# Performance work log

Measured on AMD Instinct MI355X. Metric: run time of the kernel, lower is better.

The kernel has to match this reference:

```python
import jax, jax.numpy as jnp
import numpy as np

N_EMBD = 64
N_HEAD = 8
HEAD_SIZE = N_EMBD // N_HEAD  # 8
BLOCK_SIZE = 64
B = 4096
SCALE = N_EMBD ** (-0.5)  # NOTE: source scales by C**-0.5 with C=n_embd, not head_size
EPS = 1e-5


def setup_inputs() -> dict:
    key = jax.random.key(0)
    ks = jax.random.split(key, 12)
    s = 0.02
    return {
        "x": jax.random.normal(ks[0], (B, BLOCK_SIZE, N_EMBD), jnp.float32),
        # per-head q/k/v projections packed as [C, H, hs] (no bias in source)
        "Wq": jax.random.normal(ks[1], (N_EMBD, N_HEAD, HEAD_SIZE), jnp.float32) * s,
        "Wk": jax.random.normal(ks[2], (N_EMBD, N_HEAD, HEAD_SIZE), jnp.float32) * s,
        "Wv": jax.random.normal(ks[3], (N_EMBD, N_HEAD, HEAD_SIZE), jnp.float32) * s,
        "Wo": jax.random.normal(ks[4], (N_EMBD, N_EMBD), jnp.float32) * s,
        "bo": jnp.zeros((N_EMBD,), jnp.float32),
        "W1": jax.random.normal(ks[5], (N_EMBD, 4 * N_EMBD), jnp.float32) * s,
        "b1": jnp.zeros((4 * N_EMBD,), jnp.float32),
        "W2": jax.random.normal(ks[6], (4 * N_EMBD, N_EMBD), jnp.float32) * s,
        "b2": jnp.zeros((N_EMBD,), jnp.float32),
        "g1": jnp.ones((N_EMBD,), jnp.float32),
        "be1": jnp.zeros((N_EMBD,), jnp.float32),
        "g2": jnp.ones((N_EMBD,), jnp.float32),
        "be2": jnp.zeros((N_EMBD,), jnp.float32),
    }


def _layernorm(x, g, b):
    mu = jnp.mean(x, axis=-1, keepdims=True)
    var = jnp.mean(jnp.square(x - mu), axis=-1, keepdims=True)
    return (x - mu) * jax.lax.rsqrt(var + EPS) * g + b


def reference(x, Wq, Wk, Wv, Wo, bo, W1, b1, W2, b2, g1, be1, g2, be2):
    Bb, T, C = x.shape
    # --- multi-head causal self-attention (dropout = identity in eval) ---
    h = _layernorm(x, g1, be1)
    q = jnp.einsum('btc,chd->bhtd', h, Wq)
    k = jnp.einsum('btc,chd->bhtd', h, Wk)
    v = jnp.einsum('btc,chd->bhtd', h, Wv)
    wei = jnp.einsum('bhtd,bhsd->bhts', q, k) * SCALE
    mask = jnp.tril(jnp.ones((T, T), dtype=bool))
    wei = jnp.where(mask, wei, -jnp.inf)
    wei = jax.nn.softmax(wei, axis=-1)
    attn = jnp.einsum('bhts,bhsd->bhtd', wei, v)
    attn = attn.transpose(0, 2, 1, 3).reshape(Bb, T, C)  # concat heads
    x = x + attn @ Wo + bo
    # --- feed-forward ---
    h2 = _layernorm(x, g2, be2)
    ff = jax.nn.relu(h2 @ W1 + b1) @ W2 + b2
    return x + ff
```

## Files before the change

### kernel.cpp

```cpp
#include <hip/hip_runtime.h>
#include <hip/hip_bf16.h>


typedef __attribute__((ext_vector_type(8))) short short8;
typedef __attribute__((ext_vector_type(4))) float f32x4;

#if __has_builtin(__builtin_amdgcn_exp2f)
#define EXP2F(x) __builtin_amdgcn_exp2f(x)
#else
#define EXP2F(x) __expf((x) * 0.69314718056f)
#endif
#if __has_builtin(__builtin_amdgcn_rcpf)
#define RCPF(x) __builtin_amdgcn_rcpf(x)
#else
#define RCPF(x) (1.0f / (x))
#endif

#define ST  72
#define STU 136
#define OH  0
#define OKK 4608
#define OV  9216
#define OP  13896
#define OU  4608
#define NSH 18504

__device__ __forceinline__ short f2bf(float f) {
    unsigned int u = __float_as_uint(f);
    u += 0x7fffu + ((u >> 16) & 1u);
    return (short)(u >> 16);
}
__device__ __forceinline__ unsigned pk2(float a, float b) {
    float2 t; t.x = a; t.y = b;
    __hip_bfloat162 h = __float22bfloat162_rn(t);
    unsigned u; __builtin_memcpy(&u, &h, 4); return u;
}
__device__ __forceinline__ f32x4 mfma16(short8 a, short8 b, f32x4 c) {
    return __builtin_amdgcn_mfma_f32_16x16x32_bf16(a, b, c, 0, 0, 0);
}

__global__ __launch_bounds__(64) void prepack_kernel(
    const float* __restrict__ Wq, const float* __restrict__ Wk,
    const float* __restrict__ Wv, const float* __restrict__ Wo,
    const float* __restrict__ W1, const float* __restrict__ W2,
    short* __restrict__ ws)
{
    int gid = blockIdx.x * 64 + threadIdx.x;
    int lane = gid & 63;
    int fid  = gid >> 6;
    int quad = lane >> 4, nn = lane & 15;
    short8 o;
    if (fid < 24) {
        int tile = fid >> 1, ks = fid & 1;
        const float* Ws = (tile < 4) ? Wq : ((tile < 8) ? Wk : Wv);
        float scale = (tile < 4) ? 0.18033688011f : 1.0f;
        int col = (tile & 3) * 16 + nn;
#pragma unroll
        for (int j = 0; j < 8; ++j)
            o[j] = f2bf(Ws[(ks * 32 + quad * 8 + j) * 64 + col] * scale);
    } else if (fid < 32) {
        int idx = fid - 24, nt = idx >> 1, ks = idx & 1;
#pragma unroll
        for (int j = 0; j < 8; ++j)
            o[j] = f2bf(Wo[(ks * 32 + quad * 8 + j) * 64 + nt * 16 + nn]);
    } else if (fid < 64) {
        int idx = fid - 32, c = idx >> 3, tile = (idx >> 1) & 3, ks = idx & 1;
#pragma unroll
        for (int j = 0; j < 8; ++j)
            o[j] = f2bf(W1[(ks * 32 + quad * 8 + j) * 256 + c * 64 + tile * 16 + nn]);
    } else {
        int idx = fid - 64, c = idx >> 3, nt = (idx >> 1) & 3, ks = idx & 1;
#pragma unroll
        for (int j = 0; j < 8; ++j)
            o[j] = f2bf(W2[(c * 64 + ks * 32 + quad * 8 + j) * 64 + nt * 16 + nn]);
    }
    *(short8*)(ws + (size_t)gid * 8) = o;
}

__global__ __launch_bounds__(256, 4) void block_kernel(
    const float* __restrict__ x,
    const float* __restrict__ bo,
    const float* __restrict__ b1,
    const float* __restrict__ b2,
    const float* __restrict__ g1, const float* __restrict__ be1,
    const float* __restrict__ g2, const float* __restrict__ be2,
    const short8* __restrict__ WB,
    float* __restrict__ out)
{
    __shared__ short sm[NSH];
    const int tid  = threadIdx.x;
    const int wv   = tid >> 6;
    const int lane = tid & 63;
    const int quad = lane >> 4;
    const int nn   = lane & 15;
    const int t_my = wv * 16 + nn;
    const int b    = blockIdx.x;
    const float* xb = x + (size_t)b * 4096;
    const f32x4 zf = {0.f, 0.f, 0.f, 0.f};
    const short8 z8 = {0, 0, 0, 0, 0, 0, 0, 0};

    if (tid < ST) sm[OV + 64 * ST + tid] = (short)0x3F80;
    float xr[16];
    float gv[4], bv[4];
#pragma unroll
    for (int nt = 0; nt < 4; ++nt) { gv[nt] = g1[nt * 16 + nn]; bv[nt] = be1[nt * 16 + nn]; }
#pragma unroll
    for (int nt = 0; nt < 4; ++nt)
#pragma unroll
        for (int r = 0; r < 4; ++r)
            xr[nt * 4 + r] = xb[(wv * 16 + quad * 4 + r) * 64 + nt * 16 + nn];
#pragma unroll
    for (int r = 0; r < 4; ++r) {
        float s1 = 0.f, s2 = 0.f;
#pragma unroll
        for (int nt = 0; nt < 4; ++nt) { float v = xr[nt * 4 + r]; s1 += v; s2 += v * v; }
        s1 += __shfl_xor(s1, 1); s1 += __shfl_xor(s1, 2); s1 += __shfl_xor(s1, 4); s1 += __shfl_xor(s1, 8);
        s2 += __shfl_xor(s2, 1); s2 += __shfl_xor(s2, 2); s2 += __shfl_xor(s2, 4); s2 += __shfl_xor(s2, 8);
        float mu = s1 * 0.015625f;
        float rstd = rsqrtf(s2 * 0.015625f - mu * mu + 1e-5f);
        int base = OH + (wv * 16 + quad * 4 + r) * ST + nn;
        float h0 = (xr[0 + r]  - mu) * rstd * gv[0] + bv[0];
        float h1 = (xr[4 + r]  - mu) * rstd * gv[1] + bv[1];
        float h2 = (xr[8 + r]  - mu) * rstd * gv[2] + bv[2];
        float h3 = (xr[12 + r] - mu) * rstd * gv[3] + bv[3];
        unsigned pA = pk2(h0, h1), pB = pk2(h2, h3);
        sm[base +  0] = (short)pA;
        sm[base + 16] = (short)(pA >> 16);
        sm[base + 32] = (short)pB;
        sm[base + 48] = (short)(pB >> 16);
    }
    __syncthreads();

    unsigned qp[8];
    {
        const short8 wk0 = WB[(size_t)((4 + wv) * 2 + 0) * 64 + lane];
        const short8 wk1 = WB[(size_t)((4 + wv) * 2 + 1) * 64 + lane];
        const short8 wv0 = WB[(size_t)((8 + wv) * 2 + 0) * 64 + lane];
        const short8 wv1 = WB[(size_t)((8 + wv) * 2 + 1) * 64 + lane];
        short8 hf0 = *(const short8*)&sm[OH + t_my * ST + quad * 8];
        short8 hf1 = *(const short8*)&sm[OH + t_my * ST + 32 + quad * 8];
#pragma unroll
        for (int jt = 0; jt < 4; ++jt) {
            f32x4 a = mfma16(WB[(size_t)(jt * 2 + 0) * 64 + lane], hf0, zf);
            a = mfma16(WB[(size_t)(jt * 2 + 1) * 64 + lane], hf1, a);
            qp[jt * 2 + 0] = pk2(a[0], a[1]);
            qp[jt * 2 + 1] = pk2(a[2], a[3]);
        }
#pragma unroll
        for (int rt = 0; rt < 4; ++rt) {
            short8 hA = *(const short8*)&sm[OH + (rt * 16 + nn) * ST + quad * 8];
            short8 hB = *(const short8*)&sm[OH + (rt * 16 + nn) * ST + 32 + quad * 8];
            f32x4 ka = mfma16(wk0, hA, zf); ka = mfma16(wk1, hB, ka);
            uint2 w1; w1.x = pk2(ka[0], ka[1]); w1.y = pk2(ka[2], ka[3]);
            *(uint2*)&sm[OKK + (rt * 16 + nn) * ST + wv * 16 + quad * 4] = w1;
            f32x4 va = mfma16(hA, wv0, zf); va = mfma16(hB, wv1, va);
            uint2 w2; w2.x = pk2(va[0], va[1]); w2.y = pk2(va[2], va[3]);
            *(uint2*)&sm[OV + (wv * 16 + nn) * ST + rt * 16 + quad * 4] = w2;
        }
    }
    __syncthreads();

    const bool keep0 = (quad * 4 + 0) <= nn, keep1 = (quad * 4 + 1) <= nn;
    const bool keep2 = (quad * 4 + 2) <= nn, keep3 = (quad * 4 + 3) <= nn;
    const int arow_base = (nn < 8) ? nn : 64;
    const int arow_step = (nn < 8) ? 8 : 0;
    const int nks = (wv < 2) ? 1 : 2;
    const int zhi = nks * 2;
    for (int mt = wv + 1; mt < zhi; ++mt) {
        uint2 w; w.x = 0u; w.y = 0u;
        *(uint2*)&sm[OP + t_my * ST + mt * 16 + quad * 4] = w;
    }
#pragma unroll 2
    for (int h = 0; h < 8; ++h) {
        short8 bq;
        {
            int qsA = ((h & 1) * 2) * 16 + nn, qsB = qsA + 16;
            int qi = (h >> 1) * 2;
            union { unsigned u[4]; short8 s; } bb;
            bb.u[0] = __shfl(qp[qi + 0], qsA);
            bb.u[1] = __shfl(qp[qi + 1], qsA);
            bb.u[2] = __shfl(qp[qi + 0], qsB);
            bb.u[3] = __shfl(qp[qi + 1], qsB);
            bq = bb.s;
        }
#pragma unroll
        for (int mt = 0; mt < 4; ++mt) {
            if (mt <= wv) {
                short8 ak = z8;
                if (quad == 0) ak = *(const short8*)&sm[OKK + (mt * 16 + nn) * ST + h * 8];
                f32x4 s = mfma16(ak, bq, zf);
                float e0 = EXP2F(s[0]), e1 = EXP2F(s[1]), e2 = EXP2F(s[2]), e3 = EXP2F(s[3]);
                if (mt == wv) {
                    e0 = keep0 ? e0 : 0.f; e1 = keep1 ? e1 : 0.f;
                    e2 = keep2 ? e2 : 0.f; e3 = keep3 ? e3 : 0.f;
                }
                uint2 w; w.x = pk2(e0, e1); w.y = pk2(e2, e3);
                *(uint2*)&sm[OP + t_my * ST + mt * 16 + quad * 4] = w;
            }
        }
        const int arow = arow_base + h * arow_step;
        f32x4 pv = zf;
#pragma unroll
        for (int ks = 0; ks < 2; ++ks) {
            if (ks < nks) {
                short8 av = *(const short8*)&sm[OV + arow * ST + ks * 32 + quad * 8];
                short8 bp = *(const short8*)&sm[OP + t_my * ST + ks * 32 + quad * 8];
                pv = mfma16(av, bp, pv);
            }
        }
        float denom = __shfl(pv[0], 32 + nn);
        float rd = RCPF(denom);
        if (quad < 2) {
            uint2 w; w.x = pk2(pv[0] * rd, pv[1] * rd); w.y = pk2(pv[2] * rd, pv[3] * rd);
            *(uint2*)&sm[OH + t_my * ST + h * 8 + quad * 4] = w;
        }
    }

    {
        short8 aa0 = *(const short8*)&sm[OH + t_my * ST + quad * 8];
        short8 aa1 = *(const short8*)&sm[OH + t_my * ST + 32 + quad * 8];
#pragma unroll
        for (int nt = 0; nt < 4; ++nt) {
            f32x4 oa = mfma16(aa0, WB[(size_t)(24 + nt * 2 + 0) * 64 + lane], zf);
            oa = mfma16(aa1, WB[(size_t)(24 + nt * 2 + 1) * 64 + lane], oa);
            float bov = bo[nt * 16 + nn];
#pragma unroll
            for (int r = 0; r < 4; ++r) xr[nt * 4 + r] += oa[r] + bov;
        }
    }
#pragma unroll
    for (int nt = 0; nt < 4; ++nt) { gv[nt] = g2[nt * 16 + nn]; bv[nt] = be2[nt * 16 + nn]; }
#pragma unroll
    for (int r = 0; r < 4; ++r) {
        float s1 = 0.f, s2 = 0.f;
#pragma unroll
        for (int nt = 0; nt < 4; ++nt) { float v = xr[nt * 4 + r]; s1 += v; s2 += v * v; }
        s1 += __shfl_xor(s1, 1); s1 += __shfl_xor(s1, 2); s1 += __shfl_xor(s1, 4); s1 += __shfl_xor(s1, 8);
        s2 += __shfl_xor(s2, 1); s2 += __shfl_xor(s2, 2); s2 += __shfl_xor(s2, 4); s2 += __shfl_xor(s2, 8);
        float mu = s1 * 0.015625f;
        float rstd = rsqrtf(s2 * 0.015625f - mu * mu + 1e-5f);
        int base = OP + (wv * 16 + quad * 4 + r) * ST + nn;
        float h0 = (xr[0 + r]  - mu) * rstd * gv[0] + bv[0];
        float h1 = (xr[4 + r]  - mu) * rstd * gv[1] + bv[1];
        float h2 = (xr[8 + r]  - mu) * rstd * gv[2] + bv[2];
        float h3 = (xr[12 + r] - mu) * rstd * gv[3] + bv[3];
        unsigned pA = pk2(h0, h1), pB = pk2(h2, h3);
        sm[base +  0] = (short)pA;
        sm[base + 16] = (short)(pA >> 16);
        sm[base + 32] = (short)pB;
        sm[base + 48] = (short)(pB >> 16);
    }
    __syncthreads();

    short8 h2r[4][2];
#pragma unroll
    for (int rt = 0; rt < 4; ++rt) {
        h2r[rt][0] = *(const short8*)&sm[OP + (rt * 16 + nn) * ST + quad * 8];
        h2r[rt][1] = *(const short8*)&sm[OP + (rt * 16 + nn) * ST + 32 + quad * 8];
    }
    f32x4 fa[4];
#pragma unroll
    for (int rt = 0; rt < 4; ++rt) fa[rt] = zf;
#pragma unroll
    for (int c = 0; c < 2; ++c) {
#pragma unroll
        for (int g = 0; g < 2; ++g) {
            int gc = c * 8 + wv * 2 + g;
            int fid = 32 + (gc >> 2) * 8 + (gc & 3) * 2;
            short8 wf0 = WB[(size_t)fid * 64 + lane];
            short8 wf1 = WB[(size_t)(fid + 1) * 64 + lane];
            const float4 bb = *(const float4*)&b1[gc * 16 + quad * 4];
#pragma unroll
            for (int rt = 0; rt < 4; ++rt) {
                f32x4 u = mfma16(wf0, h2r[rt][0], zf);
                u = mfma16(wf1, h2r[rt][1], u);
                float u0 = fmaxf(u[0] + bb.x, 0.f), u1 = fmaxf(u[1] + bb.y, 0.f);
                float u2 = fmaxf(u[2] + bb.z, 0.f), u3 = fmaxf(u[3] + bb.w, 0.f);
                uint2 w; w.x = pk2(u0, u1); w.y = pk2(u2, u3);
                *(uint2*)&sm[OU + (rt * 16 + nn) * STU + (wv * 2 + g) * 16 + quad * 4] = w;
            }
        }
        __syncthreads();
#pragma unroll
        for (int kl = 0; kl < 4; ++kl) {
            int fidb = 64 + (c * 2 + (kl >> 1)) * 8 + wv * 2 + (kl & 1);
            short8 w2f = WB[(size_t)fidb * 64 + lane];
#pragma unroll
            for (int rt = 0; rt < 4; ++rt) {
                short8 au = *(const short8*)&sm[OU + (rt * 16 + nn) * STU + kl * 32 + quad * 8];
                fa[rt] = mfma16(au, w2f, fa[rt]);
            }
        }
        if (c == 0) __syncthreads();
    }
    {
        float* yr = (wv < 2) ? (float*)sm : (float*)(sm + OP);
        const int ycol = (wv & 1) * 16 + nn;
#pragma unroll
        for (int rt = 0; rt < 4; ++rt)
#pragma unroll
            for (int r = 0; r < 4; ++r)
                yr[(rt * 16 + quad * 4 + r) * 34 + ycol] = fa[rt][r];
    }
    __syncthreads();

    float* ob = out + (size_t)b * 4096;
    const float* yA = (const float*)sm;
    const float* yB = (const float*)(sm + OP);
#pragma unroll
    for (int nt = 0; nt < 4; ++nt) {
        const float* ys = (nt < 2) ? yA : yB;
        float b2v = b2[nt * 16 + nn];
#pragma unroll
        for (int r = 0; r < 4; ++r) {
            float yv = ys[(wv * 16 + quad * 4 + r) * 34 + (nt & 1) * 16 + nn];
            ob[(wv * 16 + quad * 4 + r) * 64 + nt * 16 + nn] = xr[nt * 4 + r] + yv + b2v;
        }
    }
}

extern "C" void kernel_launch(void* const* d_in, const int* in_sizes, int n_in,
                              void* d_out, int out_size, void* d_ws, size_t ws_size,
                              hipStream_t stream) {
    const float* x   = (const float*)d_in[0];
    const float* Wq  = (const float*)d_in[1];
    const float* Wk  = (const float*)d_in[2];
    const float* Wv  = (const float*)d_in[3];
    const float* Wo  = (const float*)d_in[4];
    const float* bo  = (const float*)d_in[5];
    const float* W1  = (const float*)d_in[6];
    const float* b1  = (const float*)d_in[7];
    const float* W2  = (const float*)d_in[8];
    const float* b2  = (const float*)d_in[9];
    const float* g1  = (const float*)d_in[10];
    const float* be1 = (const float*)d_in[11];
    const float* g2  = (const float*)d_in[12];
    const float* be2 = (const float*)d_in[13];
    short* ws = (short*)d_ws;
    prepack_kernel<<<dim3(96), dim3(64), 0, stream>>>(Wq, Wk, Wv, Wo, W1, W2, ws);
    const int nb = in_sizes[0] / 4096;
    block_kernel<<<dim3(nb), dim3(256), 0, stream>>>(
        x, bo, b1, b2, g1, be1, g2, be2, (const short8*)ws, (float*)d_out);
}
```

Baseline: 196.9 us.

## Shrink shared memory to raise occupancy; compute softmax denominators by shuffle

Shrinks the shared-memory footprint from about 37KB to 32KB. It does this by giving the probability buffer a narrower stride and storing the final FFN output as bf16 instead of fp32. The launch bound moves to 5 blocks per CU. The softmax denominator is now summed from the exponentials with cross-lane shuffles, replacing the ones-row trick in the V matrix, so V rows are loaded only for half the lanes. The trade-off is extra bf16 rounding of the FFN output before the residual add, which reduces accuracy.

```diff
diff --git a/kernel.cpp b/kernel.cpp
--- a/kernel.cpp
+++ b/kernel.cpp
@@ -17,13 +17,14 @@
 #endif
 
 #define ST  72
+#define STP 40
 #define STU 136
 #define OH  0
 #define OKK 4608
 #define OV  9216
-#define OP  13896
+#define OP  13824
 #define OU  4608
-#define NSH 18504
+#define NSH 16384
 
 __device__ __forceinline__ short f2bf(float f) {
     unsigned int u = __float_as_uint(f);
@@ -34,6 +35,9 @@
     float2 t; t.x = a; t.y = b;
     __hip_bfloat162 h = __float22bfloat162_rn(t);
     unsigned u; __builtin_memcpy(&u, &h, 4); return u;
+}
+__device__ __forceinline__ float bf2f(short s) {
+    return __uint_as_float(((unsigned)(unsigned short)s) << 16);
 }
 __device__ __forceinline__ f32x4 mfma16(short8 a, short8 b, f32x4 c) {
     return __builtin_amdgcn_mfma_f32_16x16x32_bf16(a, b, c, 0, 0, 0);
@@ -77,7 +81,7 @@
     *(short8*)(ws + (size_t)gid * 8) = o;
 }
 
-__global__ __launch_bounds__(256, 4) void block_kernel(
+__global__ __launch_bounds__(256, 5) void block_kernel(
     const float* __restrict__ x,
     const float* __restrict__ bo,
     const float* __restrict__ b1,
@@ -99,7 +103,6 @@
     const f32x4 zf = {0.f, 0.f, 0.f, 0.f};
     const short8 z8 = {0, 0, 0, 0, 0, 0, 0, 0};
 
-    if (tid < ST) sm[OV + 64 * ST + tid] = (short)0x3F80;
     float xr[16];
     float gv[4], bv[4];
 #pragma unroll
@@ -137,15 +140,6 @@
         const short8 wk1 = WB[(size_t)((4 + wv) * 2 + 1) * 64 + lane];
         const short8 wv0 = WB[(size_t)((8 + wv) * 2 + 0) * 64 + lane];
         const short8 wv1 = WB[(size_t)((8 + wv) * 2 + 1) * 64 + lane];
-        short8 hf0 = *(const short8*)&sm[OH + t_my * ST + quad * 8];
-        short8 hf1 = *(const short8*)&sm[OH + t_my * ST + 32 + quad * 8];
-#pragma unroll
-        for (int jt = 0; jt < 4; ++jt) {
-            f32x4 a = mfma16(WB[(size_t)(jt * 2 + 0) * 64 + lane], hf0, zf);
-            a = mfma16(WB[(size_t)(jt * 2 + 1) * 64 + lane], hf1, a);
-            qp[jt * 2 + 0] = pk2(a[0], a[1]);
-            qp[jt * 2 + 1] = pk2(a[2], a[3]);
-        }
 #pragma unroll
         for (int rt = 0; rt < 4; ++rt) {
             short8 hA = *(const short8*)&sm[OH + (rt * 16 + nn) * ST + quad * 8];
@@ -157,18 +151,25 @@
             uint2 w2; w2.x = pk2(va[0], va[1]); w2.y = pk2(va[2], va[3]);
             *(uint2*)&sm[OV + (wv * 16 + nn) * ST + rt * 16 + quad * 4] = w2;
         }
+        short8 hf0 = *(const short8*)&sm[OH + t_my * ST + quad * 8];
+        short8 hf1 = *(const short8*)&sm[OH + t_my * ST + 32 + quad * 8];
+#pragma unroll
+        for (int jt = 0; jt < 4; ++jt) {
+            f32x4 a = mfma16(WB[(size_t)(jt * 2 + 0) * 64 + lane], hf0, zf);
+            a = mfma16(WB[(size_t)(jt * 2 + 1) * 64 + lane], hf1, a);
+            qp[jt * 2 + 0] = pk2(a[0], a[1]);
+            qp[jt * 2 + 1] = pk2(a[2], a[3]);
+        }
     }
     __syncthreads();
 
     const bool keep0 = (quad * 4 + 0) <= nn, keep1 = (quad * 4 + 1) <= nn;
     const bool keep2 = (quad * 4 + 2) <= nn, keep3 = (quad * 4 + 3) <= nn;
-    const int arow_base = (nn < 8) ? nn : 64;
-    const int arow_step = (nn < 8) ? 8 : 0;
     const int nks = (wv < 2) ? 1 : 2;
     const int zhi = nks * 2;
     for (int mt = wv + 1; mt < zhi; ++mt) {
         uint2 w; w.x = 0u; w.y = 0u;
-        *(uint2*)&sm[OP + t_my * ST + mt * 16 + quad * 4] = w;
+        *(uint2*)&sm[OP + t_my * STP + mt * 16 + quad * 4] = w;
     }
 #pragma unroll 2
     for (int h = 0; h < 8; ++h) {
@@ -183,6 +184,7 @@
             bb.u[3] = __shfl(qp[qi + 1], qsB);
             bq = bb.s;
         }
+        float es = 0.f;
 #pragma unroll
         for (int mt = 0; mt < 4; ++mt) {
             if (mt <= wv) {
@@ -194,22 +196,24 @@
                     e0 = keep0 ? e0 : 0.f; e1 = keep1 ? e1 : 0.f;
                     e2 = keep2 ? e2 : 0.f; e3 = keep3 ? e3 : 0.f;
                 }
+                es += (e0 + e1) + (e2 + e3);
                 uint2 w; w.x = pk2(e0, e1); w.y = pk2(e2, e3);
-                *(uint2*)&sm[OP + t_my * ST + mt * 16 + quad * 4] = w;
+                *(uint2*)&sm[OP + t_my * STP + mt * 16 + quad * 4] = w;
             }
         }
-        const int arow = arow_base + h * arow_step;
         f32x4 pv = zf;
 #pragma unroll
         for (int ks = 0; ks < 2; ++ks) {
             if (ks < nks) {
-                short8 av = *(const short8*)&sm[OV + arow * ST + ks * 32 + quad * 8];
-                short8 bp = *(const short8*)&sm[OP + t_my * ST + ks * 32 + quad * 8];
+                short8 av = z8;
+                if (nn < 8) av = *(const short8*)&sm[OV + (h * 8 + nn) * ST + ks * 32 + quad * 8];
+                short8 bp = *(const short8*)&sm[OP + t_my * STP + ks * 32 + quad * 8];
                 pv = mfma16(av, bp, pv);
             }
         }
-        float denom = __shfl(pv[0], 32 + nn);
-        float rd = RCPF(denom);
+        es += __shfl_xor(es, 16);
+        es += __shfl_xor(es, 32);
+        float rd = RCPF(es);
         if (quad < 2) {
             uint2 w; w.x = pk2(pv[0] * rd, pv[1] * rd); w.y = pk2(pv[2] * rd, pv[3] * rd);
             *(uint2*)&sm[OH + t_my * ST + h * 8 + quad * 4] = w;
@@ -239,7 +243,7 @@
         s2 += __shfl_xor(s2, 1); s2 += __shfl_xor(s2, 2); s2 += __shfl_xor(s2, 4); s2 += __shfl_xor(s2, 8);
         float mu = s1 * 0.015625f;
         float rstd = rsqrtf(s2 * 0.015625f - mu * mu + 1e-5f);
-        int base = OP + (wv * 16 + quad * 4 + r) * ST + nn;
+        int base = OH + (wv * 16 + quad * 4 + r) * ST + nn;
         float h0 = (xr[0 + r]  - mu) * rstd * gv[0] + bv[0];
         float h1 = (xr[4 + r]  - mu) * rstd * gv[1] + bv[1];
         float h2 = (xr[8 + r]  - mu) * rstd * gv[2] + bv[2];
@@ -255,8 +259,8 @@
     short8 h2r[4][2];
 #pragma unroll
     for (int rt = 0; rt < 4; ++rt) {
-        h2r[rt][0] = *(const short8*)&sm[OP + (rt * 16 + nn) * ST + quad * 8];
-        h2r[rt][1] = *(const short8*)&sm[OP + (rt * 16 + nn) * ST + 32 + quad * 8];
+        h2r[rt][0] = *(const short8*)&sm[OH + (rt * 16 + nn) * ST + quad * 8];
+        h2r[rt][1] = *(const short8*)&sm[OH + (rt * 16 + nn) * ST + 32 + quad * 8];
     }
     f32x4 fa[4];
 #pragma unroll
@@ -294,26 +298,24 @@
         if (c == 0) __syncthreads();
     }
     {
-        float* yr = (wv < 2) ? (float*)sm : (float*)(sm + OP);
+        short* yh = sm + ((wv < 2) ? OP : OH);
         const int ycol = (wv & 1) * 16 + nn;
 #pragma unroll
         for (int rt = 0; rt < 4; ++rt)
 #pragma unroll
             for (int r = 0; r < 4; ++r)
-                yr[(rt * 16 + quad * 4 + r) * 34 + ycol] = fa[rt][r];
+                yh[(rt * 16 + quad * 4 + r) * STP + ycol] = f2bf(fa[rt][r]);
     }
     __syncthreads();
 
     float* ob = out + (size_t)b * 4096;
-    const float* yA = (const float*)sm;
-    const float* yB = (const float*)(sm + OP);
 #pragma unroll
     for (int nt = 0; nt < 4; ++nt) {
-        const float* ys = (nt < 2) ? yA : yB;
+        const short* ys = sm + ((nt < 2) ? OP : OH);
         float b2v = b2[nt * 16 + nn];
 #pragma unroll
         for (int r = 0; r < 4; ++r) {
-            float yv = ys[(wv * 16 + quad * 4 + r) * 34 + (nt & 1) * 16 + nn];
+            float yv = bf2f(ys[(wv * 16 + quad * 4 + r) * STP + (nt & 1) * 16 + nn]);
             ob[(wv * 16 + quad * 4 + r) * 64 + nt * 16 + nn] = xr[nt * 4 + r] + yv + b2v;
         }
     }
```

New measurement: 234.5 us. 19.1% more time.
